# Kernel optimization log

Hardware: AMD Instinct MI355X
Metric: run time of the kernel (lower is better)

## Reference

```python
import jax, jax.numpy as jnp
import numpy as np

EPS = 1e-5

def _ln(x):
    # LayerNorm over last dim, no affine (elementwise_affine=False), biased variance
    mu = jnp.mean(x, axis=-1, keepdims=True)
    var = jnp.mean(jnp.square(x - mu), axis=-1, keepdims=True)
    return (x - mu) / jnp.sqrt(var + EPS)

def setup_inputs() -> dict:
    key = jax.random.key(0)
    B, I, H = 32768, 512, 512
    ks = jax.random.split(key, 12)
    std = 1.0 / np.sqrt(H)
    u = lambda k, shape: jax.random.uniform(k, shape, jnp.float32, -std, std)
    return {
        "x": jax.random.normal(ks[0], (B, I), jnp.float32),
        "h": jax.random.normal(ks[1], (B, H), jnp.float32),
        "W_i2h": u(ks[2], (I, 2 * H)),
        "b_i2h": u(ks[3], (2 * H,)),
        "W_h2h": u(ks[4], (H, 2 * H)),
        "b_h2h": u(ks[5], (2 * H,)),
        "W_hatW": u(ks[6], (I, H)),
        "b_hatW": u(ks[7], (H,)),
        "W_hatU": u(ks[8], (H, H)),
        "b_hatU": u(ks[9], (H,)),
    }

def reference(x, h, W_i2h, b_i2h, W_h2h, b_h2h, W_hatW, b_hatW, W_hatU, b_hatU):
    H = W_hatU.shape[0]
    i2h = _ln(x @ W_i2h + b_i2h)          # [B, 2H]
    h2h = _ln(h @ W_h2h + b_h2h)          # [B, 2H]
    gates = jax.nn.sigmoid(i2h + h2h)
    z_t = gates[:, :H]
    r_t = gates[:, -H:]
    h_hat_first = _ln(x @ W_hatW + b_hatW)  # [B, H]
    h_hat_last = _ln(h @ W_hatU + b_hatU)   # [B, H]
    h_hat = jnp.tanh(h_hat_first + r_t * h_hat_last)
    h_t = (1.0 - z_t) * h + z_t * h_hat
    return h_t
```

## Files before the change

kernel.cpp:

```cpp
#include <hip/hip_runtime.h>
#include <hip/hip_bf16.h>
#include <stdint.h>

typedef unsigned short u16;
typedef __attribute__((ext_vector_type(8))) short short8;
typedef __attribute__((ext_vector_type(4))) short short4v;
typedef __attribute__((ext_vector_type(4))) float f4;
typedef __attribute__((ext_vector_type(4))) float f32x4;

static __device__ __forceinline__ u16 f2b(float f) {
  union { float f; uint32_t u; } c; c.f = f;
  return (u16)((c.u + 0x7FFFu + ((c.u >> 16) & 1u)) >> 16);
}
static __device__ __forceinline__ float b2f(u16 s) {
  union { uint32_t u; float f; } c; c.u = ((uint32_t)s) << 16; return c.f;
}
static __device__ __forceinline__ uint32_t pk2(float lo, float hi) {
  __hip_bfloat162 b = __float22bfloat162_rn(make_float2(lo, hi));
  union { __hip_bfloat162 b; uint32_t u; } c; c.b = b; return c.u;
}

__global__ __launch_bounds__(256) void cvt_kernel(const float* __restrict__ x,
                                                  const float* __restrict__ h,
                                                  u16* __restrict__ Ab,
                                                  int rowStart, int nBlkHalf) {
  bool isH = (int)blockIdx.x >= nBlkHalf;
  int blk = isH ? (blockIdx.x - nBlkHalf) : blockIdx.x;
  const float* src = (isH ? h : x) + (size_t)rowStart * 512;
  u16* dst = Ab + (size_t)rowStart * 512 + (isH ? ((size_t)32768 * 512) : 0);
  size_t e = ((size_t)blk * 256 + threadIdx.x) << 3;

  f4 v0, v1;
  asm volatile(
      "global_load_dwordx4 %0, %2, off\n\t"
      "global_load_dwordx4 %1, %2, off offset:16\n\t"
      "s_waitcnt vmcnt(0)"
      : "=&v"(v0), "=&v"(v1)
      : "v"(src + e)
      : "memory");

  short8 o;
  o[0] = (short)f2b(v0[0]); o[1] = (short)f2b(v0[1]);
  o[2] = (short)f2b(v0[2]); o[3] = (short)f2b(v0[3]);
  o[4] = (short)f2b(v1[0]); o[5] = (short)f2b(v1[1]);
  o[6] = (short)f2b(v1[2]); o[7] = (short)f2b(v1[3]);
  *(short8*)(dst + e) = o;
}

__global__ __launch_bounds__(256) void transpose_cat(const float* __restrict__ WA0,
                                                     const float* __restrict__ WB0,
                                                     const float* __restrict__ WA1,
                                                     const float* __restrict__ WB1,
                                                     u16* __restrict__ dst0,
                                                     u16* __restrict__ dst1) {
  __shared__ float t[32][33];
  int n0 = blockIdx.x * 32, k0 = blockIdx.y * 32;
  int tx = threadIdx.x, ty = threadIdx.y;
  const float* srcA = blockIdx.z ? WA1 : WA0;
  const float* srcB = blockIdx.z ? WB1 : WB0;
  u16* dst = blockIdx.z ? dst1 : dst0;
  const float* src; int strideN, nb;
  if (n0 < 1024) { src = srcA; strideN = 1024; nb = n0; }
  else           { src = srcB; strideN = 512;  nb = n0 - 1024; }
#pragma unroll
  for (int i = 0; i < 4; ++i) {
    int k = k0 + ty + i * 8;
    t[tx][ty + i * 8] = src[(size_t)k * strideN + nb + tx];
  }
  __syncthreads();
#pragma unroll
  for (int i = 0; i < 4; ++i) {
    int n = ty + i * 8;
    dst[(size_t)(n0 + n) * 512 + k0 + tx] = f2b(t[n][tx]);
  }
}

#define AS1 __attribute__((address_space(1)))
#define AS3 __attribute__((address_space(3)))
#define SBAR0 __builtin_amdgcn_sched_barrier(0)
#define MF __builtin_amdgcn_mfma_f32_16x16x32_bf16

__global__ __launch_bounds__(512, 2) void gemm_kernel(
    const u16* __restrict__ Ab, const u16* __restrict__ WxT,
    const u16* __restrict__ WhT, u16* __restrict__ Cb,
    int rowStartX, int rowStartH, int tilesPerHalf) {
  __shared__ u16 lds[65536];

  int tid = threadIdx.x, lane = tid & 63, wv = tid >> 6;
  int wm = wv >> 2, wn = wv & 3;
  int l15 = lane & 15, l4 = lane >> 4, l7 = lane & 7;

  int nwg = gridDim.x, bid = blockIdx.x;
  int swz = (nwg & 7) ? bid : ((bid & 7) * (nwg >> 3) + (bid >> 3));
  int mb = swz / 6, nb = swz - mb * 6;
  size_t m0; const u16* Wt;
  if (mb < tilesPerHalf) { m0 = (size_t)rowStartX + (size_t)mb * 256; Wt = WxT; }
  else { m0 = (size_t)rowStartH + (size_t)(mb - tilesPerHalf) * 256; Wt = WhT; }
  int crow0 = mb * 256, n0 = nb * 256;
  const u16* At = Ab + m0 * 512;
  const u16* Bt = Wt + (size_t)n0 * 512;

#define UNIT(tbase, row0, kt, dstoff) do { \
    _Pragma("unroll") \
    for (int i_ = 0; i_ < 2; ++i_) { \
      int si_ = i_ * 512 + tid; \
      int r_ = si_ >> 3, s_ = si_ & 7; \
      int g_ = s_ ^ (r_ & 7); \
      __builtin_amdgcn_global_load_lds( \
          (const AS1 void*)((tbase) + (size_t)((row0) + r_) * 512 + (kt) * 64 + g_ * 8), \
          (AS3 void*)(lds + (dstoff) + si_ * 8), 16, 0, 0); \
    } \
  } while (0)

#define LDA(bufo, q, mr, ks) \
  (*(const short8*)(lds + (bufo) + (wm * 128 + (q) * 32 + (mr) * 16 + l15) * 64 + \
                    ((((ks) * 4 + l4) ^ l7) << 3)))
#define LDB(bufo, f, ks) \
  (*(const short8*)(lds + (bufo) + 16384 + (wn * 64 + (f) * 16 + l15) * 64 + \
                    ((((ks) * 4 + l4) ^ l7) << 3)))

#define BARSEQ do { SBAR0; __builtin_amdgcn_s_barrier(); \
    asm volatile("s_waitcnt lgkmcnt(0)" ::: "memory"); SBAR0; } while (0)

#define MFMAQ(q, A00, A10, A01, A11) do { \
    __builtin_amdgcn_s_setprio(1); \
    _Pragma("unroll") for (int f_ = 0; f_ < 4; ++f_) \
      acc[(q)*2][f_]   = MF(br[f_][0], A00, acc[(q)*2][f_], 0, 0, 0); \
    _Pragma("unroll") for (int f_ = 0; f_ < 4; ++f_) \
      acc[(q)*2+1][f_] = MF(br[f_][0], A10, acc[(q)*2+1][f_], 0, 0, 0); \
    _Pragma("unroll") for (int f_ = 0; f_ < 4; ++f_) \
      acc[(q)*2][f_]   = MF(br[f_][1], A01, acc[(q)*2][f_], 0, 0, 0); \
    _Pragma("unroll") for (int f_ = 0; f_ < 4; ++f_) \
      acc[(q)*2+1][f_] = MF(br[f_][1], A11, acc[(q)*2+1][f_], 0, 0, 0); \
    __builtin_amdgcn_s_setprio(0); \
  } while (0)

#define PH(bufo, q) \
    short8 a00 = LDA(bufo, q, 0, 0), a10 = LDA(bufo, q, 1, 0), \
           a01 = LDA(bufo, q, 0, 1), a11 = LDA(bufo, q, 1, 1)

  f32x4 acc[8][4] = {};

  UNIT(At, 0,   0, 0);     UNIT(At, 128, 0, 8192);
  UNIT(Bt, 0,   0, 16384); UNIT(Bt, 128, 0, 24576);
  UNIT(Bt, 0,   1, 32768 + 16384); UNIT(Bt, 128, 1, 32768 + 24576);
  asm volatile("s_waitcnt vmcnt(4)" ::: "memory");
  SBAR0; __builtin_amdgcn_s_barrier(); SBAR0;

#pragma unroll
  for (int t = 0; t < 4; ++t) {
    const int b0 = 0, b1 = 32768;
    const int k1 = 2 * t + 1;
    const bool st = (t < 3);
    short8 br[4][2];
    {
#pragma unroll
      for (int f_ = 0; f_ < 4; ++f_) { br[f_][0] = LDB(b0, f_, 0); br[f_][1] = LDB(b0, f_, 1); }
      PH(b0, 0);
      UNIT(At, 0, k1, b1 + 0);
      BARSEQ; MFMAQ(0, a00, a10, a01, a11);
    }
    {
      PH(b0, 1);
      UNIT(At, 128, k1, b1 + 8192);
      BARSEQ; MFMAQ(1, a00, a10, a01, a11);
    }
    {
      PH(b0, 2);
      if (st) UNIT(Bt, 0, k1 + 1, b0 + 16384);
      BARSEQ; MFMAQ(2, a00, a10, a01, a11);
    }
    {
      PH(b0, 3);
      if (st) { UNIT(Bt, 128, k1 + 1, b0 + 24576);
                asm volatile("s_waitcnt vmcnt(4)" ::: "memory"); }
      else    { asm volatile("s_waitcnt vmcnt(0)" ::: "memory"); }
      BARSEQ; MFMAQ(3, a00, a10, a01, a11);
    }
    {
#pragma unroll
      for (int f_ = 0; f_ < 4; ++f_) { br[f_][0] = LDB(b1, f_, 0); br[f_][1] = LDB(b1, f_, 1); }
      PH(b1, 0);
      if (st) UNIT(At, 0, k1 + 1, b0 + 0);
      BARSEQ; MFMAQ(0, a00, a10, a01, a11);
    }
    {
      PH(b1, 1);
      if (st) UNIT(At, 128, k1 + 1, b0 + 8192);
      BARSEQ; MFMAQ(1, a00, a10, a01, a11);
    }
    {
      PH(b1, 2);
      if (st) UNIT(Bt, 0, k1 + 2, b1 + 16384);
      BARSEQ; MFMAQ(2, a00, a10, a01, a11);
    }
    {
      PH(b1, 3);
      if (st) { UNIT(Bt, 128, k1 + 2, b1 + 24576);
                asm volatile("s_waitcnt vmcnt(4)" ::: "memory"); }
      BARSEQ; MFMAQ(3, a00, a10, a01, a11);
    }
  }
#undef UNIT
#undef LDA
#undef LDB
#undef BARSEQ
#undef MFMAQ
#undef PH

  const int TP = 264;
#pragma unroll
  for (int pass = 0; pass < 2; ++pass) {
    SBAR0; __builtin_amdgcn_s_barrier(); SBAR0;
    if (wm == pass) {
#pragma unroll
      for (int mr = 0; mr < 8; ++mr) {
        int ml = mr * 16 + l15;
#pragma unroll
        for (int nr = 0; nr < 4; ++nr) {
          int c4 = wn * 16 + nr * 4 + l4;
          uint2 w;
          w.x = pk2(acc[mr][nr][0], acc[mr][nr][1]);
          w.y = pk2(acc[mr][nr][2], acc[mr][nr][3]);
          *(uint2*)(lds + ml * TP + c4 * 4) = w;
        }
      }
    }
    SBAR0; __builtin_amdgcn_s_barrier(); SBAR0;
    int row = tid >> 2;
    int q = tid & 3;
    size_t gbase = (size_t)(crow0 + pass * 128 + row) * 1536 + n0;
#pragma unroll
    for (int j = 0; j < 8; ++j) {
      int c8 = q + 4 * j;
      short8 v = *(const short8*)(lds + row * TP + c8 * 8);
      *(short8*)(Cb + gbase + c8 * 8) = v;
    }
  }
}

__global__ __launch_bounds__(256) void epi_kernel(
    const u16* __restrict__ Cb, const float* __restrict__ h,
    const float* __restrict__ b_i2h, const float* __restrict__ b_h2h,
    const float* __restrict__ b_hatW, const float* __restrict__ b_hatU,
    float* __restrict__ out, int mBase, int BC) {
  int wv = threadIdx.x >> 6;
  int lane = threadIdx.x & 63;
  int mLocal = blockIdx.x * 4 + wv;
  size_t mGlob = (size_t)mBase + mLocal;
  const u16* Ar = Cb + (size_t)mLocal * 1536;
  const u16* Br = Cb + ((size_t)BC + mLocal) * 1536;
  int j0 = lane * 8;

  float a[3][8], b[3][8];
#pragma unroll
  for (int c = 0; c < 3; ++c) {
    short8 va = *(const short8*)(Ar + c * 512 + j0);
    short8 vb = *(const short8*)(Br + c * 512 + j0);
    const float* biasA = (c == 0) ? (b_i2h + j0) : (c == 1) ? (b_i2h + 512 + j0) : (b_hatW + j0);
    const float* biasB = (c == 0) ? (b_h2h + j0) : (c == 1) ? (b_h2h + 512 + j0) : (b_hatU + j0);
    f4 ba0 = *(const f4*)biasA, ba1 = *(const f4*)(biasA + 4);
    f4 bb0 = *(const f4*)biasB, bb1 = *(const f4*)(biasB + 4);
#pragma unroll
    for (int j = 0; j < 4; ++j) {
      a[c][j]     = b2f((u16)va[j])     + ba0[j];
      a[c][j + 4] = b2f((u16)va[j + 4]) + ba1[j];
      b[c][j]     = b2f((u16)vb[j])     + bb0[j];
      b[c][j + 4] = b2f((u16)vb[j + 4]) + bb1[j];
    }
  }

  float s1a = 0, q1a = 0, s2a = 0, q2a = 0, s1b = 0, q1b = 0, s2b = 0, q2b = 0;
#pragma unroll
  for (int j = 0; j < 8; ++j) {
    s1a += a[0][j] + a[1][j]; q1a += a[0][j] * a[0][j] + a[1][j] * a[1][j];
    s2a += a[2][j];           q2a += a[2][j] * a[2][j];
    s1b += b[0][j] + b[1][j]; q1b += b[0][j] * b[0][j] + b[1][j] * b[1][j];
    s2b += b[2][j];           q2b += b[2][j] * b[2][j];
  }
#pragma unroll
  for (int off = 32; off > 0; off >>= 1) {
    s1a += __shfl_xor(s1a, off); q1a += __shfl_xor(q1a, off);
    s2a += __shfl_xor(s2a, off); q2a += __shfl_xor(q2a, off);
    s1b += __shfl_xor(s1b, off); q1b += __shfl_xor(q1b, off);
    s2b += __shfl_xor(s2b, off); q2b += __shfl_xor(q2b, off);
  }
  const float inv1 = 1.0f / 1024.0f, inv2 = 1.0f / 512.0f, eps = 1e-5f;
  float mu1a = s1a * inv1, mu2a = s2a * inv2, mu1b = s1b * inv1, mu2b = s2b * inv2;
  float rs1a = rsqrtf(q1a * inv1 - mu1a * mu1a + eps);
  float rs2a = rsqrtf(q2a * inv2 - mu2a * mu2a + eps);
  float rs1b = rsqrtf(q1b * inv1 - mu1b * mu1b + eps);
  float rs2b = rsqrtf(q2b * inv2 - mu2b * mu2b + eps);

  const float* hrow = h + mGlob * 512 + j0;
  f4 h0 = *(const f4*)hrow, h1 = *(const f4*)(hrow + 4);
  f4 o0, o1;
#pragma unroll
  for (int j = 0; j < 8; ++j) {
    float zs  = (a[0][j] - mu1a) * rs1a + (b[0][j] - mu1b) * rs1b;
    float rsg = (a[1][j] - mu1a) * rs1a + (b[1][j] - mu1b) * rs1b;
    float z = 1.0f / (1.0f + __expf(-zs));
    float r = 1.0f / (1.0f + __expf(-rsg));
    float hh = tanhf((a[2][j] - mu2a) * rs2a + r * ((b[2][j] - mu2b) * rs2b));
    float hv = (j < 4) ? h0[j] : h1[j - 4];
    float o = hv + z * (hh - hv);
    if (j < 4) o0[j] = o; else o1[j - 4] = o;
  }
  *(f4*)(out + mGlob * 512 + j0) = o0;
  *(f4*)(out + mGlob * 512 + j0 + 4) = o1;
}

extern "C" void kernel_launch(void* const* d_in, const int* in_sizes, int n_in,
                              void* d_out, int out_size, void* d_ws, size_t ws_size,
                              hipStream_t stream) {
  const float* x      = (const float*)d_in[0];
  const float* h      = (const float*)d_in[1];
  const float* W_i2h  = (const float*)d_in[2];
  const float* b_i2h  = (const float*)d_in[3];
  const float* W_h2h  = (const float*)d_in[4];
  const float* b_h2h  = (const float*)d_in[5];
  const float* W_hatW = (const float*)d_in[6];
  const float* b_hatW = (const float*)d_in[7];
  const float* W_hatU = (const float*)d_in[8];
  const float* b_hatU = (const float*)d_in[9];
  float* out = (float*)d_out;

  u16* WxT = (u16*)d_ws;
  u16* WhT = WxT + (size_t)1536 * 512;
  u16* Ab  = WhT + (size_t)1536 * 512;
  u16* Cb  = Ab + (size_t)65536 * 512;

  size_t fixedElems = (size_t)2 * 1536 * 512 + (size_t)65536 * 512;
  int chunks = 2;
  for (;;) {
    size_t need = (fixedElems + (size_t)2 * (32768 / chunks) * 1536) * sizeof(u16);
    if (need <= ws_size || chunks >= 128) break;
    chunks <<= 1;
  }
  int BC = 32768 / chunks;
  int tph = BC / 256;
  int nwg = 2 * tph * 6;
  int nBlkHalf = BC / 4;

  transpose_cat<<<dim3(48, 16, 2), dim3(32, 8), 0, stream>>>(
      W_i2h, W_hatW, W_h2h, W_hatU, WxT, WhT);
  for (int cc = 0; cc < chunks; ++cc) {
    cvt_kernel<<<2 * nBlkHalf, 256, 0, stream>>>(x, h, Ab, cc * BC, nBlkHalf);
    gemm_kernel<<<nwg, 512, 0, stream>>>(Ab, WxT, WhT, Cb,
                                         cc * BC, 32768 + cc * BC, tph);
    epi_kernel<<<BC / 4, 256, 0, stream>>>(Cb, h, b_i2h, b_h2h, b_hatW, b_hatU,
                                           out, cc * BC, BC);
  }
}
```

Measured before the change: 214.7 us.

## Fuse fp32-to-bf16 activation conversion into GEMM A-tile loads

Removes the separate conversion kernel and its bf16 scratch buffer. The GEMM now loads fp32 x/h rows into registers, converts them to bf16 in-kernel, and writes the swizzled values to LDS, staggered across the pipeline phases. This saves a full write and re-read of the bf16 activation copy and one launch per chunk. In exchange the kernel needs more registers, reads fp32 A twice (once per N tile group), and adds extra LDS-write waits before the barriers.

```diff
diff --git a/kernel.cpp b/kernel.cpp
--- a/kernel.cpp
+++ b/kernel.cpp
@@ -18,33 +18,6 @@
 static __device__ __forceinline__ uint32_t pk2(float lo, float hi) {
   __hip_bfloat162 b = __float22bfloat162_rn(make_float2(lo, hi));
   union { __hip_bfloat162 b; uint32_t u; } c; c.b = b; return c.u;
-}
-
-__global__ __launch_bounds__(256) void cvt_kernel(const float* __restrict__ x,
-                                                  const float* __restrict__ h,
-                                                  u16* __restrict__ Ab,
-                                                  int rowStart, int nBlkHalf) {
-  bool isH = (int)blockIdx.x >= nBlkHalf;
-  int blk = isH ? (blockIdx.x - nBlkHalf) : blockIdx.x;
-  const float* src = (isH ? h : x) + (size_t)rowStart * 512;
-  u16* dst = Ab + (size_t)rowStart * 512 + (isH ? ((size_t)32768 * 512) : 0);
-  size_t e = ((size_t)blk * 256 + threadIdx.x) << 3;
-
-  f4 v0, v1;
-  asm volatile(
-      "global_load_dwordx4 %0, %2, off\n\t"
-      "global_load_dwordx4 %1, %2, off offset:16\n\t"
-      "s_waitcnt vmcnt(0)"
-      : "=&v"(v0), "=&v"(v1)
-      : "v"(src + e)
-      : "memory");
-
-  short8 o;
-  o[0] = (short)f2b(v0[0]); o[1] = (short)f2b(v0[1]);
-  o[2] = (short)f2b(v0[2]); o[3] = (short)f2b(v0[3]);
-  o[4] = (short)f2b(v1[0]); o[5] = (short)f2b(v1[1]);
-  o[6] = (short)f2b(v1[2]); o[7] = (short)f2b(v1[3]);
-  *(short8*)(dst + e) = o;
 }
 
 __global__ __launch_bounds__(256) void transpose_cat(const float* __restrict__ WA0,
@@ -81,9 +54,9 @@
 #define MF __builtin_amdgcn_mfma_f32_16x16x32_bf16
 
 __global__ __launch_bounds__(512, 2) void gemm_kernel(
-    const u16* __restrict__ Ab, const u16* __restrict__ WxT,
-    const u16* __restrict__ WhT, u16* __restrict__ Cb,
-    int rowStartX, int rowStartH, int tilesPerHalf) {
+    const float* __restrict__ X, const float* __restrict__ Hm,
+    const u16* __restrict__ WxT, const u16* __restrict__ WhT,
+    u16* __restrict__ Cb, int rowStart, int tilesPerHalf) {
   __shared__ u16 lds[65536];
 
   int tid = threadIdx.x, lane = tid & 63, wv = tid >> 6;
@@ -93,21 +66,47 @@
   int nwg = gridDim.x, bid = blockIdx.x;
   int swz = (nwg & 7) ? bid : ((bid & 7) * (nwg >> 3) + (bid >> 3));
   int mb = swz / 6, nb = swz - mb * 6;
-  size_t m0; const u16* Wt;
-  if (mb < tilesPerHalf) { m0 = (size_t)rowStartX + (size_t)mb * 256; Wt = WxT; }
-  else { m0 = (size_t)rowStartH + (size_t)(mb - tilesPerHalf) * 256; Wt = WhT; }
+  const float* Af; const u16* Wt;
+  if (mb < tilesPerHalf) {
+    Af = X + (size_t)(rowStart + mb * 256) * 512; Wt = WxT;
+  } else {
+    Af = Hm + (size_t)(rowStart + (mb - tilesPerHalf) * 256) * 512; Wt = WhT;
+  }
   int crow0 = mb * 256, n0 = nb * 256;
-  const u16* At = Ab + m0 * 512;
   const u16* Bt = Wt + (size_t)n0 * 512;
 
-#define UNIT(tbase, row0, kt, dstoff) do { \
+  int ar = tid >> 2;
+  int ak = (tid & 3) << 4;
+  int s0 = (tid & 3) * 2;
+  int r7 = ar & 7;
+  const float* aBase = Af + (size_t)ar * 512 + ak;
+  int aw0 = ar * 64 + ((s0 ^ r7) << 3);
+  int aw1 = ar * 64 + (((s0 + 1) ^ r7) << 3);
+
+#define ALOADF(v, row0, kt) do { \
+    const float* p_ = aBase + (size_t)(row0) * 512 + ((kt) << 6); \
+    v##0 = *(const f4*)(p_);     v##1 = *(const f4*)(p_ + 4); \
+    v##2 = *(const f4*)(p_ + 8); v##3 = *(const f4*)(p_ + 12); \
+  } while (0)
+
+#define AWRITE(v, dstoff) do { \
+    uint4 w0_, w1_; \
+    w0_.x = pk2(v##0[0], v##0[1]); w0_.y = pk2(v##0[2], v##0[3]); \
+    w0_.z = pk2(v##1[0], v##1[1]); w0_.w = pk2(v##1[2], v##1[3]); \
+    w1_.x = pk2(v##2[0], v##2[1]); w1_.y = pk2(v##2[2], v##2[3]); \
+    w1_.z = pk2(v##3[0], v##3[1]); w1_.w = pk2(v##3[2], v##3[3]); \
+    *(uint4*)(lds + (dstoff) + aw0) = w0_; \
+    *(uint4*)(lds + (dstoff) + aw1) = w1_; \
+  } while (0)
+
+#define UNIT(row0, kt, dstoff) do { \
     _Pragma("unroll") \
     for (int i_ = 0; i_ < 2; ++i_) { \
       int si_ = i_ * 512 + tid; \
       int r_ = si_ >> 3, s_ = si_ & 7; \
       int g_ = s_ ^ (r_ & 7); \
       __builtin_amdgcn_global_load_lds( \
-          (const AS1 void*)((tbase) + (size_t)((row0) + r_) * 512 + (kt) * 64 + g_ * 8), \
+          (const AS1 void*)(Bt + (size_t)((row0) + r_) * 512 + (kt) * 64 + g_ * 8), \
           (AS3 void*)(lds + (dstoff) + si_ * 8), 16, 0, 0); \
     } \
   } while (0)
@@ -120,6 +119,10 @@
                     ((((ks) * 4 + l4) ^ l7) << 3)))
 
 #define BARSEQ do { SBAR0; __builtin_amdgcn_s_barrier(); \
+    asm volatile("s_waitcnt lgkmcnt(0)" ::: "memory"); SBAR0; } while (0)
+#define BARSEQW do { SBAR0; \
+    asm volatile("s_waitcnt lgkmcnt(0)" ::: "memory"); \
+    __builtin_amdgcn_s_barrier(); \
     asm volatile("s_waitcnt lgkmcnt(0)" ::: "memory"); SBAR0; } while (0)
 
 #define MFMAQ(q, A00, A10, A01, A11) do { \
@@ -140,12 +143,19 @@
            a01 = LDA(bufo, q, 0, 1), a11 = LDA(bufo, q, 1, 1)
 
   f32x4 acc[8][4] = {};
-
-  UNIT(At, 0,   0, 0);     UNIT(At, 128, 0, 8192);
-  UNIT(Bt, 0,   0, 16384); UNIT(Bt, 128, 0, 24576);
-  UNIT(Bt, 0,   1, 32768 + 16384); UNIT(Bt, 128, 1, 32768 + 24576);
+  f4 al0, al1, al2, al3, ah0, ah1, ah2, ah3;
+
+  ALOADF(al, 0, 0);
+  ALOADF(ah, 128, 0);
+  UNIT(0,   0, 16384); UNIT(128, 0, 24576);
+  UNIT(0,   1, 32768 + 16384); UNIT(128, 1, 32768 + 24576);
+  AWRITE(al, 0);
+  AWRITE(ah, 8192);
   asm volatile("s_waitcnt vmcnt(4)" ::: "memory");
-  SBAR0; __builtin_amdgcn_s_barrier(); SBAR0;
+  SBAR0;
+  asm volatile("s_waitcnt lgkmcnt(0)" ::: "memory");
+  __builtin_amdgcn_s_barrier();
+  SBAR0;
 
 #pragma unroll
   for (int t = 0; t < 4; ++t) {
@@ -157,54 +167,59 @@
 #pragma unroll
       for (int f_ = 0; f_ < 4; ++f_) { br[f_][0] = LDB(b0, f_, 0); br[f_][1] = LDB(b0, f_, 1); }
       PH(b0, 0);
-      UNIT(At, 0, k1, b1 + 0);
+      ALOADF(al, 0, k1);
       BARSEQ; MFMAQ(0, a00, a10, a01, a11);
     }
     {
       PH(b0, 1);
-      UNIT(At, 128, k1, b1 + 8192);
+      ALOADF(ah, 128, k1);
       BARSEQ; MFMAQ(1, a00, a10, a01, a11);
     }
     {
       PH(b0, 2);
-      if (st) UNIT(Bt, 0, k1 + 1, b0 + 16384);
-      BARSEQ; MFMAQ(2, a00, a10, a01, a11);
+      if (st) UNIT(0, k1 + 1, b0 + 16384);
+      AWRITE(al, b1 + 0);
+      BARSEQW; MFMAQ(2, a00, a10, a01, a11);
     }
     {
       PH(b0, 3);
-      if (st) { UNIT(Bt, 128, k1 + 1, b0 + 24576);
-                asm volatile("s_waitcnt vmcnt(4)" ::: "memory"); }
+      if (st) UNIT(128, k1 + 1, b0 + 24576);
+      AWRITE(ah, b1 + 8192);
+      if (st) { asm volatile("s_waitcnt vmcnt(4)" ::: "memory"); }
       else    { asm volatile("s_waitcnt vmcnt(0)" ::: "memory"); }
-      BARSEQ; MFMAQ(3, a00, a10, a01, a11);
+      BARSEQW; MFMAQ(3, a00, a10, a01, a11);
     }
     {
 #pragma unroll
       for (int f_ = 0; f_ < 4; ++f_) { br[f_][0] = LDB(b1, f_, 0); br[f_][1] = LDB(b1, f_, 1); }
       PH(b1, 0);
-      if (st) UNIT(At, 0, k1 + 1, b0 + 0);
+      if (st) ALOADF(al, 0, k1 + 1);
       BARSEQ; MFMAQ(0, a00, a10, a01, a11);
     }
     {
       PH(b1, 1);
-      if (st) UNIT(At, 128, k1 + 1, b0 + 8192);
+      if (st) ALOADF(ah, 128, k1 + 1);
       BARSEQ; MFMAQ(1, a00, a10, a01, a11);
     }
     {
       PH(b1, 2);
-      if (st) UNIT(Bt, 0, k1 + 2, b1 + 16384);
-      BARSEQ; MFMAQ(2, a00, a10, a01, a11);
+      if (st) { UNIT(0, k1 + 2, b1 + 16384); AWRITE(al, b0 + 0); }
+      BARSEQW; MFMAQ(2, a00, a10, a01, a11);
     }
     {
       PH(b1, 3);
-      if (st) { UNIT(Bt, 128, k1 + 2, b1 + 24576);
+      if (st) { UNIT(128, k1 + 2, b1 + 24576); AWRITE(ah, b0 + 8192);
                 asm volatile("s_waitcnt vmcnt(4)" ::: "memory"); }
-      BARSEQ; MFMAQ(3, a00, a10, a01, a11);
-    }
-  }
+      BARSEQW; MFMAQ(3, a00, a10, a01, a11);
+    }
+  }
+#undef ALOADF
+#undef AWRITE
 #undef UNIT
 #undef LDA
 #undef LDB
 #undef BARSEQ
+#undef BARSEQW
 #undef MFMAQ
 #undef PH
 
@@ -226,6 +241,7 @@
         }
       }
     }
+    asm volatile("s_waitcnt lgkmcnt(0)" ::: "memory");
     SBAR0; __builtin_amdgcn_s_barrier(); SBAR0;
     int row = tid >> 2;
     int q = tid & 3;
@@ -327,10 +343,9 @@
 
   u16* WxT = (u16*)d_ws;
   u16* WhT = WxT + (size_t)1536 * 512;
-  u16* Ab  = WhT + (size_t)1536 * 512;
-  u16* Cb  = Ab + (size_t)65536 * 512;
-
-  size_t fixedElems = (size_t)2 * 1536 * 512 + (size_t)65536 * 512;
+  u16* Cb  = WhT + (size_t)1536 * 512;
+
+  size_t fixedElems = (size_t)2 * 1536 * 512;
   int chunks = 2;
   for (;;) {
     size_t need = (fixedElems + (size_t)2 * (32768 / chunks) * 1536) * sizeof(u16);
@@ -340,14 +355,11 @@
   int BC = 32768 / chunks;
   int tph = BC / 256;
   int nwg = 2 * tph * 6;
-  int nBlkHalf = BC / 4;
 
   transpose_cat<<<dim3(48, 16, 2), dim3(32, 8), 0, stream>>>(
       W_i2h, W_hatW, W_h2h, W_hatU, WxT, WhT);
   for (int cc = 0; cc < chunks; ++cc) {
-    cvt_kernel<<<2 * nBlkHalf, 256, 0, stream>>>(x, h, Ab, cc * BC, nBlkHalf);
-    gemm_kernel<<<nwg, 512, 0, stream>>>(Ab, WxT, WhT, Cb,
-                                         cc * BC, 32768 + cc * BC, tph);
+    gemm_kernel<<<nwg, 512, 0, stream>>>(x, h, WxT, WhT, Cb, cc * BC, tph);
     epi_kernel<<<BC / 4, 256, 0, stream>>>(Cb, h, b_i2h, b_h2h, b_hatW, b_hatU,
                                            out, cc * BC, BC);
   }
```

Result: slower. 263.4 us (+22.7%).

## Restructure GEMM pipeline to triple-buffered A with single B buffer

Applied to the files above, without the earlier changes.

Changes the GEMM LDS schedule from a double-buffered A/B layout with two K-steps per iteration to an eight-iteration loop. A rotates through three LDS buffers and B uses a single buffer that is reloaded each step. Intent is to prefetch A two steps ahead and issue loads earlier relative to the MFMA work. It also replaces the bf16 packing intrinsic with a manual rounding routine, adds an lgkmcnt wait before the epilogue barrier, and starts the chunk search at one chunk so fewer kernel launches are needed when workspace allows. Rewriting the single B buffer in place relies on barrier ordering and may add stalls.

```diff
diff --git a/kernel.cpp b/kernel.cpp
--- a/kernel.cpp
+++ b/kernel.cpp
@@ -1,5 +1,4 @@
 #include <hip/hip_runtime.h>
-#include <hip/hip_bf16.h>
 #include <stdint.h>
 
 typedef unsigned short u16;
@@ -14,10 +13,6 @@
 }
 static __device__ __forceinline__ float b2f(u16 s) {
   union { uint32_t u; float f; } c; c.u = ((uint32_t)s) << 16; return c.f;
-}
-static __device__ __forceinline__ uint32_t pk2(float lo, float hi) {
-  __hip_bfloat162 b = __float22bfloat162_rn(make_float2(lo, hi));
-  union { __hip_bfloat162 b; uint32_t u; } c; c.b = b; return c.u;
 }
 
 __global__ __launch_bounds__(256) void cvt_kernel(const float* __restrict__ x,
@@ -112,11 +107,11 @@
     } \
   } while (0)
 
-#define LDA(bufo, q, mr, ks) \
-  (*(const short8*)(lds + (bufo) + (wm * 128 + (q) * 32 + (mr) * 16 + l15) * 64 + \
+#define LDA(aoff, q, mr, ks) \
+  (*(const short8*)(lds + (aoff) + (wm * 128 + (q) * 32 + (mr) * 16 + l15) * 64 + \
                     ((((ks) * 4 + l4) ^ l7) << 3)))
-#define LDB(bufo, f, ks) \
-  (*(const short8*)(lds + (bufo) + 16384 + (wn * 64 + (f) * 16 + l15) * 64 + \
+#define LDB(f, ks) \
+  (*(const short8*)(lds + 49152 + (wn * 64 + (f) * 16 + l15) * 64 + \
                     ((((ks) * 4 + l4) ^ l7) << 3)))
 
 #define BARSEQ do { SBAR0; __builtin_amdgcn_s_barrier(); \
@@ -135,69 +130,45 @@
     __builtin_amdgcn_s_setprio(0); \
   } while (0)
 
-#define PH(bufo, q) \
-    short8 a00 = LDA(bufo, q, 0, 0), a10 = LDA(bufo, q, 1, 0), \
-           a01 = LDA(bufo, q, 0, 1), a11 = LDA(bufo, q, 1, 1)
+#define PH(aoff, q) \
+    short8 a00 = LDA(aoff, q, 0, 0), a10 = LDA(aoff, q, 1, 0), \
+           a01 = LDA(aoff, q, 0, 1), a11 = LDA(aoff, q, 1, 1)
 
   f32x4 acc[8][4] = {};
 
-  UNIT(At, 0,   0, 0);     UNIT(At, 128, 0, 8192);
-  UNIT(Bt, 0,   0, 16384); UNIT(Bt, 128, 0, 24576);
-  UNIT(Bt, 0,   1, 32768 + 16384); UNIT(Bt, 128, 1, 32768 + 24576);
+  UNIT(At, 0, 0, 0);      UNIT(At, 128, 0, 8192);
+  UNIT(Bt, 0, 0, 49152);  UNIT(Bt, 128, 0, 57344);
+  UNIT(At, 0, 1, 16384);  UNIT(At, 128, 1, 24576);
   asm volatile("s_waitcnt vmcnt(4)" ::: "memory");
   SBAR0; __builtin_amdgcn_s_barrier(); SBAR0;
 
 #pragma unroll
-  for (int t = 0; t < 4; ++t) {
-    const int b0 = 0, b1 = 32768;
-    const int k1 = 2 * t + 1;
-    const bool st = (t < 3);
+  for (int t = 0; t < 8; ++t) {
+    const int aoff = (t % 3) * 16384;
+    const int awr  = ((t + 2) % 3) * 16384;
     short8 br[4][2];
     {
 #pragma unroll
-      for (int f_ = 0; f_ < 4; ++f_) { br[f_][0] = LDB(b0, f_, 0); br[f_][1] = LDB(b0, f_, 1); }
-      PH(b0, 0);
-      UNIT(At, 0, k1, b1 + 0);
+      for (int f_ = 0; f_ < 4; ++f_) { br[f_][0] = LDB(f_, 0); br[f_][1] = LDB(f_, 1); }
+      PH(aoff, 0);
       BARSEQ; MFMAQ(0, a00, a10, a01, a11);
     }
     {
-      PH(b0, 1);
-      UNIT(At, 128, k1, b1 + 8192);
+      PH(aoff, 1);
+      if (t < 7) UNIT(Bt, 0, t + 1, 49152);
       BARSEQ; MFMAQ(1, a00, a10, a01, a11);
     }
     {
-      PH(b0, 2);
-      if (st) UNIT(Bt, 0, k1 + 1, b0 + 16384);
+      PH(aoff, 2);
+      if (t < 7) UNIT(Bt, 128, t + 1, 57344);
+      if (t < 6) UNIT(At, 0, t + 2, awr);
       BARSEQ; MFMAQ(2, a00, a10, a01, a11);
     }
     {
-      PH(b0, 3);
-      if (st) { UNIT(Bt, 128, k1 + 1, b0 + 24576);
-                asm volatile("s_waitcnt vmcnt(4)" ::: "memory"); }
-      else    { asm volatile("s_waitcnt vmcnt(0)" ::: "memory"); }
-      BARSEQ; MFMAQ(3, a00, a10, a01, a11);
-    }
-    {
-#pragma unroll
-      for (int f_ = 0; f_ < 4; ++f_) { br[f_][0] = LDB(b1, f_, 0); br[f_][1] = LDB(b1, f_, 1); }
-      PH(b1, 0);
-      if (st) UNIT(At, 0, k1 + 1, b0 + 0);
-      BARSEQ; MFMAQ(0, a00, a10, a01, a11);
-    }
-    {
-      PH(b1, 1);
-      if (st) UNIT(At, 128, k1 + 1, b0 + 8192);
-      BARSEQ; MFMAQ(1, a00, a10, a01, a11);
-    }
-    {
-      PH(b1, 2);
-      if (st) UNIT(Bt, 0, k1 + 2, b1 + 16384);
-      BARSEQ; MFMAQ(2, a00, a10, a01, a11);
-    }
-    {
-      PH(b1, 3);
-      if (st) { UNIT(Bt, 128, k1 + 2, b1 + 24576);
-                asm volatile("s_waitcnt vmcnt(4)" ::: "memory"); }
+      PH(aoff, 3);
+      if (t < 6) { UNIT(At, 128, t + 2, awr + 8192);
+                   asm volatile("s_waitcnt vmcnt(4)" ::: "memory"); }
+      else       { asm volatile("s_waitcnt vmcnt(0)" ::: "memory"); }
       BARSEQ; MFMAQ(3, a00, a10, a01, a11);
     }
   }
@@ -220,12 +191,13 @@
         for (int nr = 0; nr < 4; ++nr) {
           int c4 = wn * 16 + nr * 4 + l4;
           uint2 w;
-          w.x = pk2(acc[mr][nr][0], acc[mr][nr][1]);
-          w.y = pk2(acc[mr][nr][2], acc[mr][nr][3]);
+          w.x = (uint32_t)f2b(acc[mr][nr][0]) | ((uint32_t)f2b(acc[mr][nr][1]) << 16);
+          w.y = (uint32_t)f2b(acc[mr][nr][2]) | ((uint32_t)f2b(acc[mr][nr][3]) << 16);
           *(uint2*)(lds + ml * TP + c4 * 4) = w;
         }
       }
     }
+    asm volatile("s_waitcnt lgkmcnt(0)" ::: "memory");
     SBAR0; __builtin_amdgcn_s_barrier(); SBAR0;
     int row = tid >> 2;
     int q = tid & 3;
@@ -331,7 +303,7 @@
   u16* Cb  = Ab + (size_t)65536 * 512;
 
   size_t fixedElems = (size_t)2 * 1536 * 512 + (size_t)65536 * 512;
-  int chunks = 2;
+  int chunks = 1;
   for (;;) {
     size_t need = (fixedElems + (size_t)2 * (32768 / chunks) * 1536) * sizeof(u16);
     if (need <= ws_size || chunks >= 128) break;
```

Measured after the change: 220.8 us. 2.9% more time.
